# Kernel tuning notes

Measured on AMD Instinct MI355X. Metric: run time of the kernel, lower is better.

The kernel has to match this reference:

```python
import jax, jax.numpy as jnp
import numpy as np

B, T, D, H, O = 64, 2048, 256, 256, 256


def setup_inputs() -> dict:
    key = jax.random.key(0)
    ks = jax.random.split(key, 4)
    s_d = float(1.0 / np.sqrt(D))
    s_h = float(1.0 / np.sqrt(H))
    return {
        "x": jax.random.normal(ks[0], (B, T, D), jnp.float32),
        "c0": jnp.zeros((B, H), jnp.float32),
        "h0": jnp.zeros((B, H), jnp.float32),
        "Wih": jax.random.normal(ks[1], (D, 4 * H), jnp.float32) * s_d,
        "Whh": jax.random.normal(ks[2], (H, 4 * H), jnp.float32) * s_h,
        "bh": jnp.zeros((4 * H,), jnp.float32),
        "Wout": jax.random.normal(ks[3], (H, O), jnp.float32) * s_h,
        "bout": jnp.zeros((O,), jnp.float32),
    }


def reference(x, c0, h0, Wih, Whh, bh, Wout, bout):
    # Teacher-forcing OneToManyRNN: LSTM cell + Dense projection each step.
    # Gate order (flax LSTMCell): i, f, g, o.
    def step(carry, xt):
        c, h = carry
        gates = xt @ Wih + h @ Whh + bh  # [B, 4H]
        i, f, g, o = jnp.split(gates, 4, axis=-1)
        i = jax.nn.sigmoid(i)
        f = jax.nn.sigmoid(f)
        g = jnp.tanh(g)
        o = jax.nn.sigmoid(o)
        c_new = f * c + i * g
        h_new = o * jnp.tanh(c_new)
        y = h_new @ Wout + bout  # dense_out projection
        return (c_new, h_new), y

    xs = jnp.swapaxes(x, 0, 1)  # [T, B, D]
    _, ys = jax.lax.scan(step, (c0, h0), xs)
    return jnp.swapaxes(ys, 0, 1)  # [B, T, O] (stacked per-step outputs)
```

## Files before the change

### kernel.cpp

```cpp
#include <hip/hip_runtime.h>
#include <hip/hip_fp16.h>
#include <cstdint>
#include <cstddef>

typedef _Float16 half_t;
typedef _Float16 half2_t __attribute__((ext_vector_type(2)));
typedef _Float16 half8_t __attribute__((ext_vector_type(8)));
typedef float    f32x4   __attribute__((ext_vector_type(4)));
typedef unsigned int uint4v __attribute__((ext_vector_type(4)));

#define T_FULL  2048
#define T_CH    512
#define N_CHUNK 4
#define B_SZ    64
#define H_SZ    256
#define G4      1024
#define CH_M    (B_SZ * T_CH)

#define KP_RF   48
#define KP_LDS  9
#define KP_STR  7

static constexpr size_t OFF_XW   = 0;
static constexpr size_t OFF_H    = OFF_XW   + (size_t)CH_M * G4 * 2;
static constexpr size_t OFF_WIH  = OFF_H    + (size_t)CH_M * H_SZ * 2;
static constexpr size_t OFF_WOUT = OFF_WIH  + (size_t)G4 * 256 * 2;
static constexpr size_t OFF_WRF  = OFF_WOUT + (size_t)256 * 256 * 2;
static constexpr size_t OFF_WLDS = OFF_WRF  + (size_t)2 * KP_RF * 256 * 16;
static constexpr size_t OFF_WSTR = OFF_WLDS + (size_t)2 * KP_LDS * 256 * 16;
static constexpr size_t OFF_SC   = OFF_WSTR + (size_t)2 * KP_STR * 256 * 16;
static constexpr size_t OFF_SH   = OFF_SC   + (size_t)B_SZ * H_SZ * 4;

__device__ __forceinline__ unsigned int packh2(float a, float b) {
    half2_t h; h.x = (half_t)a; h.y = (half_t)b;
    return __builtin_bit_cast(unsigned int, h);
}

__device__ __forceinline__ float dot2f(unsigned int hp, unsigned int wp, float acc) {
#if __has_builtin(__builtin_amdgcn_fdot2)
    return __builtin_amdgcn_fdot2(__builtin_bit_cast(half2_t, hp),
                                  __builtin_bit_cast(half2_t, wp), acc, false);
#else
    half2_t h = __builtin_bit_cast(half2_t, hp);
    half2_t w = __builtin_bit_cast(half2_t, wp);
    return fmaf((float)h.y, (float)w.y, fmaf((float)h.x, (float)w.x, acc));
#endif
}

__device__ __forceinline__ unsigned int rlane(unsigned int v, int lane) {
    return (unsigned int)__builtin_amdgcn_readlane((int)v, lane);
}

__device__ __forceinline__ float sigm(float x)  { return 1.0f / (1.0f + __expf(-x)); }
__device__ __forceinline__ float tanh_(float x) { return 1.0f - 2.0f / (__expf(2.0f * x) + 1.0f); }

static constexpr int PACK_TOTAL = 262144 + 65536
                                + 2 * KP_RF  * 256 * 4
                                + 2 * KP_LDS * 256 * 4
                                + 2 * KP_STR * 256 * 4
                                + 16384 + 8192;

__global__ __launch_bounds__(256) void pack_kernel(
    const float* __restrict__ Wih, const float* __restrict__ Whh,
    const float* __restrict__ Wout, const float* __restrict__ c0,
    const float* __restrict__ h0,
    half_t* __restrict__ wih_t, half_t* __restrict__ wout_t,
    unsigned int* __restrict__ whh_rf, unsigned int* __restrict__ whh_lds,
    unsigned int* __restrict__ whh_str,
    float* __restrict__ state_c, unsigned int* __restrict__ state_h)
{
    const int stride = gridDim.x * blockDim.x;
    for (int idx = blockIdx.x * blockDim.x + threadIdx.x; idx < PACK_TOTAL; idx += stride) {
        int r = idx;
        if (r < 262144) {
            int n = r >> 8, k = r & 255;
            wih_t[r] = (half_t)Wih[k * 1024 + n];
            continue;
        }
        r -= 262144;
        if (r < 65536) {
            int n = r >> 8, k = r & 255;
            wout_t[r] = (half_t)Wout[k * 256 + n];
            continue;
        }
        r -= 65536;
        if (r < 2 * KP_RF * 256 * 4) {
            int j = r & 3, e = (r >> 2) & 255, q = r >> 10;
            int pl = q % KP_RF, hh = q / KP_RF;
            int k0 = 2 * (hh * 64 + pl);
            int col = j * 256 + e;
            whh_rf[r] = packh2(Whh[k0 * 1024 + col], Whh[(k0 + 1) * 1024 + col]);
            continue;
        }
        r -= 2 * KP_RF * 256 * 4;
        if (r < 2 * KP_LDS * 256 * 4) {
            int j = r & 3, e = (r >> 2) & 255, q = r >> 10;
            int ql = q % KP_LDS, hh = q / KP_LDS;
            int k0 = 2 * (hh * 64 + KP_RF + ql);
            int col = j * 256 + e;
            whh_lds[r] = packh2(Whh[k0 * 1024 + col], Whh[(k0 + 1) * 1024 + col]);
            continue;
        }
        r -= 2 * KP_LDS * 256 * 4;
        if (r < 2 * KP_STR * 256 * 4) {
            int j = r & 3, e = (r >> 2) & 255, q = r >> 10;
            int sl = q % KP_STR, hh = q / KP_STR;
            int k0 = 2 * (hh * 64 + KP_RF + KP_LDS + sl);
            int col = j * 256 + e;
            whh_str[r] = packh2(Whh[k0 * 1024 + col], Whh[(k0 + 1) * 1024 + col]);
            continue;
        }
        r -= 2 * KP_STR * 256 * 4;
        if (r < 16384) { state_c[r] = c0[r]; continue; }
        r -= 16384;
        state_h[r] = packh2(h0[2 * r], h0[2 * r + 1]);
    }
}

template<int AMODE, int CMODE>
__global__ __launch_bounds__(256) void gemm16(
    const void* __restrict__ Ap, const half_t* __restrict__ Bt,
    void* __restrict__ Cp, const float* __restrict__ bias, int chunk0)
{
    __shared__ half_t Als[128][40];
    __shared__ half_t Bls[128][40];
    const int tid  = threadIdx.x;
    const int lane = tid & 63, wid = tid >> 6;
    const int wr = wid >> 1, wc = wid & 1;
    const int m0 = blockIdx.x * 128, n0 = blockIdx.y * 128;

    f32x4 acc[4][4] = {};

    for (int kc = 0; kc < 8; ++kc) {
        __syncthreads();
        if (AMODE == 1) {
            const float* A = (const float*)Ap;
            #pragma unroll
            for (int i = 0; i < 4; ++i) {
                int l = tid + i * 256;
                int row = l >> 3, kq = l & 7;
                int m = m0 + row;
                int arow = ((m >> 9) << 11) + chunk0 + (m & 511);
                f32x4 v = *(const f32x4*)(A + (size_t)arow * 256 + kc * 32 + kq * 4);
                uint2 pk;
                pk.x = packh2(v.x, v.y);
                pk.y = packh2(v.z, v.w);
                *reinterpret_cast<uint2*>(&Als[row][kq * 4]) = pk;
            }
        } else {
            const half_t* A = (const half_t*)Ap;
            #pragma unroll
            for (int i = 0; i < 2; ++i) {
                int l = tid + i * 256;
                int row = l >> 2, ko = l & 3;
                half8_t v = *(const half8_t*)(A + (size_t)(m0 + row) * 256 + kc * 32 + ko * 8);
                *reinterpret_cast<half8_t*>(&Als[row][ko * 8]) = v;
            }
        }
        #pragma unroll
        for (int i = 0; i < 2; ++i) {
            int l = tid + i * 256;
            int row = l >> 2, ko = l & 3;
            half8_t v = *(const half8_t*)(Bt + (size_t)(n0 + row) * 256 + kc * 32 + ko * 8);
            *reinterpret_cast<half8_t*>(&Bls[row][ko * 8]) = v;
        }
        __syncthreads();

        half8_t af[4], bf[4];
        #pragma unroll
        for (int mi = 0; mi < 4; ++mi)
            af[mi] = *reinterpret_cast<const half8_t*>(&Als[wr * 64 + mi * 16 + (lane & 15)][(lane >> 4) * 8]);
        #pragma unroll
        for (int ni = 0; ni < 4; ++ni)
            bf[ni] = *reinterpret_cast<const half8_t*>(&Bls[wc * 64 + ni * 16 + (lane & 15)][(lane >> 4) * 8]);
        #pragma unroll
        for (int mi = 0; mi < 4; ++mi)
            #pragma unroll
            for (int ni = 0; ni < 4; ++ni)
                acc[mi][ni] = __builtin_amdgcn_mfma_f32_16x16x32_f16(af[mi], bf[ni], acc[mi][ni], 0, 0, 0);
    }

    #pragma unroll
    for (int mi = 0; mi < 4; ++mi) {
        #pragma unroll
        for (int ni = 0; ni < 4; ++ni) {
            #pragma unroll
            for (int reg = 0; reg < 4; ++reg) {
                int row = m0 + wr * 64 + mi * 16 + (lane >> 4) * 4 + reg;
                int col = n0 + wc * 64 + ni * 16 + (lane & 15);
                float v = acc[mi][ni][reg] + bias[col];
                if (CMODE == 0) {
                    ((half_t*)Cp)[(size_t)row * 1024 + ((col & 255) << 2) + (col >> 8)] = (half_t)v;
                } else {
                    int crow = ((row >> 9) << 11) + chunk0 + (row & 511);
                    ((float*)Cp)[(size_t)crow * 256 + col] = v;
                }
            }
        }
    }
}

#define W_A(F) F(0) F(1) F(2) F(3) F(4) F(5) F(6) F(7) F(8) F(9) F(10) F(11) \
               F(12) F(13) F(14) F(15) F(16) F(17) F(18) F(19) F(20) F(21) F(22) F(23)
#define W_B(F) F(24) F(25) F(26) F(27) F(28) F(29) F(30) F(31) F(32) F(33) F(34) F(35) \
               F(36) F(37) F(38) F(39) F(40) F(41) F(42) F(43) F(44) F(45) F(46) F(47)
#define W_ALL(F) W_A(F) W_B(F)

#define LDW(i)  uint4v w##i = wq[(i) * 256];
#define PINW(i) asm volatile("" : "+v"(w##i));
#define DOTW(i) { unsigned int s = rlane(hv, (i)); \
    a0 = dot2f(s, w##i.x, a0); a1 = dot2f(s, w##i.y, a1); \
    a2 = dot2f(s, w##i.z, a2); a3 = dot2f(s, w##i.w, a3); }
#define DOTQ(i, q) { unsigned int s = rlane(hv, KP_RF + (i)); \
    a0 = dot2f(s, (q).x, a0); a1 = dot2f(s, (q).y, a1); \
    a2 = dot2f(s, (q).z, a2); a3 = dot2f(s, (q).w, a3); }
#define DOTS(i, q) { unsigned int s = rlane(hv, KP_RF + KP_LDS + (i)); \
    a0 = dot2f(s, (q).x, a0); a1 = dot2f(s, (q).y, a1); \
    a2 = dot2f(s, (q).z, a2); a3 = dot2f(s, (q).w, a3); }

__global__ __launch_bounds__(512, 2) void rnn_kernel(
    const uint4v* __restrict__ whh_rf,
    const uint4v* __restrict__ whh_ldsrc,
    const uint4v* __restrict__ whh_str,
    const half_t* __restrict__ xw,
    half_t* __restrict__ h_out,
    float* __restrict__ state_c,
    unsigned int* __restrict__ state_h)
{
    __shared__ uint4v lds_w[2 * KP_LDS * 256];
    __shared__ f32x4  gbuf[256];
    __shared__ unsigned int hbuf[128];

    const int t    = threadIdx.x;
    const int e    = t & 255;
    const int hh   = t >> 8;
    const int lane = t & 63;
    const int b    = blockIdx.x;

    for (int i = t; i < 2 * KP_LDS * 256; i += 512) lds_w[i] = whh_ldsrc[i];
    if (t < 128) hbuf[t] = state_h[b * 128 + t];
    float c = (hh == 0) ? state_c[b * 256 + e] : 0.0f;

    const uint4v* wq = whh_rf + (size_t)hh * (KP_RF * 256) + e;
    W_ALL(LDW)
    W_ALL(PINW)
    __syncthreads();

    const half_t* xwp = xw + (size_t)b * T_CH * 1024 + e * 4;
    half_t* hop = h_out + (size_t)b * T_CH * 256 + e;
    const uint4v* strp = whh_str + hh * (KP_STR * 256) + e;
    const uint4v* ldp  = lds_w + hh * (KP_LDS * 256) + e;

    for (int step = 0; step < T_CH; ++step) {
        unsigned int hv = hbuf[hh * 64 + lane];

        uint2 xv; xv.x = 0; xv.y = 0;
        if (hh == 0) xv = *(const uint2*)xwp;

        float a0 = 0.f, a1 = 0.f, a2 = 0.f, a3 = 0.f;

        {
            uint4v t0 = strp[0],   t1 = strp[256],  t2 = strp[512],  t3 = strp[768];
            uint4v q0 = ldp[0],    q1 = ldp[256],   q2 = ldp[512],   q3 = ldp[768];

            W_A(DOTW)

            DOTQ(0, q0) DOTQ(1, q1) DOTQ(2, q2) DOTQ(3, q3)
            DOTS(0, t0) DOTS(1, t1) DOTS(2, t2) DOTS(3, t3)
        }

        {
            uint4v t4 = strp[1024], t5 = strp[1280], t6 = strp[1536];
            uint4v q4 = ldp[1024],  q5 = ldp[1280],  q6 = ldp[1536], q7 = ldp[1792];
            uint4v q8 = ldp[2048];

            W_B(DOTW)

            DOTQ(4, q4) DOTQ(5, q5) DOTQ(6, q6) DOTQ(7, q7) DOTQ(8, q8)
            DOTS(4, t4) DOTS(5, t5) DOTS(6, t6)
        }

        if (hh) {
            f32x4 p; p[0] = a0; p[1] = a1; p[2] = a2; p[3] = a3;
            gbuf[e] = p;
        }
        __syncthreads();

        half_t h16 = (half_t)0.f;
        if (hh == 0) {
            f32x4 p = gbuf[e];
            half2_t x0 = __builtin_bit_cast(half2_t, xv.x);
            half2_t x1 = __builtin_bit_cast(half2_t, xv.y);
            a0 += p[0] + (float)x0.x;
            a1 += p[1] + (float)x0.y;
            a2 += p[2] + (float)x1.x;
            a3 += p[3] + (float)x1.y;
            float ig = sigm(a0), fg = sigm(a1), gg = tanh_(a2), og = sigm(a3);
            c = fg * c + ig * gg;
            float hn = og * tanh_(c);
            h16 = (half_t)hn;
            reinterpret_cast<half_t*>(hbuf)[e] = h16;
        }
        xwp += 1024;
        __syncthreads();

        if (hh == 0) *hop = h16;
        hop += 256;
    }

    if (hh == 0) state_c[b * 256 + e] = c;
    if (t < 128) state_h[b * 128 + t] = hbuf[t];
}

extern "C" void kernel_launch(void* const* d_in, const int* in_sizes, int n_in,
                              void* d_out, int out_size, void* d_ws, size_t ws_size,
                              hipStream_t stream) {
    const float* x    = (const float*)d_in[0];
    const float* c0   = (const float*)d_in[1];
    const float* h0   = (const float*)d_in[2];
    const float* Wih  = (const float*)d_in[3];
    const float* Whh  = (const float*)d_in[4];
    const float* bh   = (const float*)d_in[5];
    const float* Wout = (const float*)d_in[6];
    const float* bout = (const float*)d_in[7];

    char* ws = (char*)d_ws;
    half_t* xw             = (half_t*)(ws + OFF_XW);
    half_t* h_chunk        = (half_t*)(ws + OFF_H);
    half_t* wih_t          = (half_t*)(ws + OFF_WIH);
    half_t* wout_t         = (half_t*)(ws + OFF_WOUT);
    unsigned int* whh_rf   = (unsigned int*)(ws + OFF_WRF);
    unsigned int* whh_lds  = (unsigned int*)(ws + OFF_WLDS);
    unsigned int* whh_str  = (unsigned int*)(ws + OFF_WSTR);
    float* state_c         = (float*)(ws + OFF_SC);
    unsigned int* state_h  = (unsigned int*)(ws + OFF_SH);

    pack_kernel<<<512, 256, 0, stream>>>(Wih, Whh, Wout, c0, h0,
                                         wih_t, wout_t, whh_rf, whh_lds, whh_str,
                                         state_c, state_h);

    for (int ch = 0; ch < N_CHUNK; ++ch) {
        int chunk0 = ch * T_CH;
        gemm16<1, 0><<<dim3(CH_M / 128, G4 / 128), 256, 0, stream>>>(
            (const void*)x, wih_t, (void*)xw, bh, chunk0);
        rnn_kernel<<<B_SZ, 512, 0, stream>>>((const uint4v*)(ws + OFF_WRF),
                                             (const uint4v*)(ws + OFF_WLDS),
                                             (const uint4v*)(ws + OFF_WSTR),
                                             xw, h_chunk, state_c, state_h);
        gemm16<0, 1><<<dim3(CH_M / 128, H_SZ / 128), 256, 0, stream>>>(
            (const void*)h_chunk, wout_t, d_out, bout, chunk0);
    }
    (void)in_sizes; (void)n_in; (void)out_size; (void)ws_size;
}
```

Baseline: 4.158 ms.

## Rebalance recurrent weight split across registers, LDS and streamed global memory

Changes how the recurrent weight matrix is split between register-resident, LDS-resident and streamed-from-global portions, moving from 48/9/7 to 36/16/12 packed K-pairs per half. The streamed portion is re-laid out so each thread reads its rows contiguously instead of with a 256-element stride. Launch bounds are replaced with explicit amdgpu attributes. Fewer pinned registers should relieve register pressure or spilling. In exchange each step does more LDS traffic and more global (likely L2) reads, which may lengthen the serial per-step critical path.

```diff
diff --git a/kernel.cpp b/kernel.cpp
--- a/kernel.cpp
+++ b/kernel.cpp
@@ -17,9 +17,9 @@
 #define G4      1024
 #define CH_M    (B_SZ * T_CH)
 
-#define KP_RF   48
-#define KP_LDS  9
-#define KP_STR  7
+#define KP_RF   36
+#define KP_LDS  16
+#define KP_STR  12
 
 static constexpr size_t OFF_XW   = 0;
 static constexpr size_t OFF_H    = OFF_XW   + (size_t)CH_M * G4 * 2;
@@ -28,7 +28,7 @@
 static constexpr size_t OFF_WRF  = OFF_WOUT + (size_t)256 * 256 * 2;
 static constexpr size_t OFF_WLDS = OFF_WRF  + (size_t)2 * KP_RF * 256 * 16;
 static constexpr size_t OFF_WSTR = OFF_WLDS + (size_t)2 * KP_LDS * 256 * 16;
-static constexpr size_t OFF_SC   = OFF_WSTR + (size_t)2 * KP_STR * 256 * 16;
+static constexpr size_t OFF_SC   = OFF_WSTR + (size_t)2 * 256 * KP_STR * 16;
 static constexpr size_t OFF_SH   = OFF_SC   + (size_t)B_SZ * H_SZ * 4;
 
 __device__ __forceinline__ unsigned int packh2(float a, float b) {
@@ -103,8 +103,9 @@
         }
         r -= 2 * KP_LDS * 256 * 4;
         if (r < 2 * KP_STR * 256 * 4) {
-            int j = r & 3, e = (r >> 2) & 255, q = r >> 10;
-            int sl = q % KP_STR, hh = q / KP_STR;
+            int j = r & 3, q = r >> 2;
+            int sl = q % KP_STR, t2 = q / KP_STR;
+            int e = t2 & 255, hh = t2 >> 8;
             int k0 = 2 * (hh * 64 + KP_RF + KP_LDS + sl);
             int col = j * 256 + e;
             whh_str[r] = packh2(Whh[k0 * 1024 + col], Whh[(k0 + 1) * 1024 + col]);
@@ -201,9 +202,9 @@
 }
 
 #define W_A(F) F(0) F(1) F(2) F(3) F(4) F(5) F(6) F(7) F(8) F(9) F(10) F(11) \
-               F(12) F(13) F(14) F(15) F(16) F(17) F(18) F(19) F(20) F(21) F(22) F(23)
-#define W_B(F) F(24) F(25) F(26) F(27) F(28) F(29) F(30) F(31) F(32) F(33) F(34) F(35) \
-               F(36) F(37) F(38) F(39) F(40) F(41) F(42) F(43) F(44) F(45) F(46) F(47)
+               F(12) F(13) F(14) F(15) F(16) F(17)
+#define W_B(F) F(18) F(19) F(20) F(21) F(22) F(23) F(24) F(25) F(26) F(27) F(28) F(29) \
+               F(30) F(31) F(32) F(33) F(34) F(35)
 #define W_ALL(F) W_A(F) W_B(F)
 
 #define LDW(i)  uint4v w##i = wq[(i) * 256];
@@ -218,7 +219,9 @@
     a0 = dot2f(s, (q).x, a0); a1 = dot2f(s, (q).y, a1); \
     a2 = dot2f(s, (q).z, a2); a3 = dot2f(s, (q).w, a3); }
 
-__global__ __launch_bounds__(512, 2) void rnn_kernel(
+__global__
+__attribute__((amdgpu_flat_work_group_size(512, 512), amdgpu_waves_per_eu(2, 2)))
+void rnn_kernel(
     const uint4v* __restrict__ whh_rf,
     const uint4v* __restrict__ whh_ldsrc,
     const uint4v* __restrict__ whh_str,
@@ -248,7 +251,7 @@
 
     const half_t* xwp = xw + (size_t)b * T_CH * 1024 + e * 4;
     half_t* hop = h_out + (size_t)b * T_CH * 256 + e;
-    const uint4v* strp = whh_str + hh * (KP_STR * 256) + e;
+    const uint4v* strq = whh_str + ((size_t)hh * 256 + e) * KP_STR;
     const uint4v* ldp  = lds_w + hh * (KP_LDS * 256) + e;
 
     for (int step = 0; step < T_CH; ++step) {
@@ -260,24 +263,31 @@
         float a0 = 0.f, a1 = 0.f, a2 = 0.f, a3 = 0.f;
 
         {
-            uint4v t0 = strp[0],   t1 = strp[256],  t2 = strp[512],  t3 = strp[768];
-            uint4v q0 = ldp[0],    q1 = ldp[256],   q2 = ldp[512],   q3 = ldp[768];
+            uint4v q0 = ldp[0],    q1 = ldp[256],  q2 = ldp[512],  q3 = ldp[768];
+            uint4v q4 = ldp[1024], q5 = ldp[1280], q6 = ldp[1536], q7 = ldp[1792];
+            uint4v t0 = strq[0], t1 = strq[1], t2 = strq[2];
+            uint4v t3 = strq[3], t4 = strq[4], t5 = strq[5];
 
             W_A(DOTW)
 
             DOTQ(0, q0) DOTQ(1, q1) DOTQ(2, q2) DOTQ(3, q3)
-            DOTS(0, t0) DOTS(1, t1) DOTS(2, t2) DOTS(3, t3)
+            DOTQ(4, q4) DOTQ(5, q5) DOTQ(6, q6) DOTQ(7, q7)
+            DOTS(0, t0) DOTS(1, t1) DOTS(2, t2)
+            DOTS(3, t3) DOTS(4, t4) DOTS(5, t5)
         }
 
         {
-            uint4v t4 = strp[1024], t5 = strp[1280], t6 = strp[1536];
-            uint4v q4 = ldp[1024],  q5 = ldp[1280],  q6 = ldp[1536], q7 = ldp[1792];
-            uint4v q8 = ldp[2048];
+            uint4v q8  = ldp[2048], q9  = ldp[2304], q10 = ldp[2560], q11 = ldp[2816];
+            uint4v q12 = ldp[3072], q13 = ldp[3328], q14 = ldp[3584], q15 = ldp[3840];
+            uint4v t6 = strq[6], t7 = strq[7], t8 = strq[8];
+            uint4v t9 = strq[9], t10 = strq[10], t11 = strq[11];
 
             W_B(DOTW)
 
-            DOTQ(4, q4) DOTQ(5, q5) DOTQ(6, q6) DOTQ(7, q7) DOTQ(8, q8)
-            DOTS(4, t4) DOTS(5, t5) DOTS(6, t6)
+            DOTQ(8, q8)   DOTQ(9, q9)   DOTQ(10, q10) DOTQ(11, q11)
+            DOTQ(12, q12) DOTQ(13, q13) DOTQ(14, q14) DOTQ(15, q15)
+            DOTS(6, t6)   DOTS(7, t7)   DOTS(8, t8)
+            DOTS(9, t9)   DOTS(10, t10) DOTS(11, t11)
         }
 
         if (hh) {
```

Measured after the change: 4.257 ms. 2.4% more time.
